# Optimization experiments

Hardware: AMD Instinct MI355X
Metric: run time of the kernel (lower is better)

## Reference

```python
import jax, jax.numpy as jnp
import numpy as np

K = 5          # retrieval_k
EPS = 1e-8     # torch cosine_similarity eps


def setup_inputs() -> dict:
    key = jax.random.key(0)
    ks = jax.random.split(key, 10)
    B, M, D, H = 1024, 65536, 384, 384
    return {
        "query": jax.random.normal(ks[0], (B, D), jnp.float32),
        "mem_vectors": jax.random.normal(ks[1], (M, D), jnp.float32),
        "coords": jax.random.normal(ks[2], (M, 2), jnp.float32),
        "spatial_weights": jax.random.normal(ks[3], (H, 2), jnp.float32),
        "W_ih": jax.random.normal(ks[4], (H, D), jnp.float32) * 0.05,
        "b_ih": jax.random.normal(ks[5], (H,), jnp.float32) * 0.05,
        "W_hh": jax.random.normal(ks[6], (H, H), jnp.float32) * 0.05,
        "b_hh": jax.random.normal(ks[7], (H,), jnp.float32) * 0.05,
        "W_g": jax.random.normal(ks[8], (H, D), jnp.float32) * 0.05,
        "b_g": jax.random.normal(ks[9], (H,), jnp.float32) * 0.05,
    }


def reference(query, mem_vectors, coords, spatial_weights,
              W_ih, b_ih, W_hh, b_hh, W_g, b_g):
    # --- spatial_activation: 1/(1+dist) from coords to mean of spatial_weights ---
    center = spatial_weights.mean(axis=0)                      # [2]
    dists = jnp.linalg.norm(coords - center, axis=1)           # [M]
    activations = 1.0 / (1.0 + dists)                          # [M]

    # --- retrieve_memories: cosine similarity + spatial activation, top-k ---
    qn = jnp.linalg.norm(query, axis=1, keepdims=True)         # [B,1]
    mn = jnp.linalg.norm(mem_vectors, axis=1, keepdims=True)   # [M,1]
    dots = query @ mem_vectors.T                               # [B,M]
    sim = dots / jnp.maximum(qn * mn.T, EPS)                   # cosine w/ torch eps
    total_sim = sim + activations[None, :]                     # [B,M]
    _, topk_idx = jax.lax.top_k(total_sim, K)                  # [B,K]
    retrieved = mem_vectors[topk_idx]                          # [B,K,D]

    # --- contextualize: tiny RNN over [query, retrieved...] then gated mix ---
    seq = jnp.concatenate([query[:, None, :], retrieved], axis=1)  # [B,K+1,D]
    x_proj = jnp.einsum('btd,hd->bth', seq, W_ih) + b_ih           # [B,K+1,H]

    def step(h, x_t):  # x_t: [B,H]
        h = jnp.tanh(x_t + h @ W_hh.T + b_hh)
        return h, None

    h0 = jnp.zeros((query.shape[0], W_hh.shape[0]), query.dtype)
    h, _ = jax.lax.scan(step, h0, jnp.swapaxes(x_proj, 0, 1))      # [B,H]

    gate = jax.nn.sigmoid(query @ W_g.T + b_g)                     # [B,H]
    direct = query @ W_ih.T + b_ih                                 # [B,H]
    return gate * h + (1.0 - gate) * direct
```

## Files before the change

kernel.cpp:

```cpp
#include <hip/hip_runtime.h>
#include <math.h>

namespace {

typedef float f32x4 __attribute__((ext_vector_type(4)));
typedef float f32x16 __attribute__((ext_vector_type(16)));
typedef short bf16x8 __attribute__((ext_vector_type(8)));
typedef unsigned short ushort_t;

constexpr int B  = 1024;
constexpr int M  = 65536;
constexpr int D  = 384;
constexpr int H  = 384;
constexpr int KK = 5;
constexpr int NC = 128;
constexpr int CHUNK = M / NC;
constexpr float FEPS = 1e-8f;

__device__ __forceinline__ ushort_t f2bf(float x) {
  unsigned int u = __float_as_uint(x);
  unsigned int r = (u + 0x7FFFu + ((u >> 16) & 1u)) >> 16;
  return (ushort_t)r;
}
__device__ __forceinline__ float bf2f(ushort_t h) {
  return __uint_as_float(((unsigned int)h) << 16);
}

__device__ __forceinline__ void async16(const ushort_t* g, ushort_t* l) {
  __builtin_amdgcn_global_load_lds(
      (const __attribute__((address_space(1))) unsigned int*)g,
      (__attribute__((address_space(3))) unsigned int*)l, 16, 0, 0);
}

__device__ __forceinline__ void insert3b(unsigned int* k, unsigned int v) {
  unsigned int t0 = min(k[0], v); k[0] = max(k[0], v);
  unsigned int t1 = min(k[1], t0); k[1] = max(k[1], t0);
  k[2] = max(k[2], t1);
}
__device__ __forceinline__ void insert5b(unsigned int* k, unsigned int v) {
  unsigned int t0 = min(k[0], v); k[0] = max(k[0], v);
  unsigned int t1 = min(k[1], t0); k[1] = max(k[1], t0);
  unsigned int t2 = min(k[2], t1); k[2] = max(k[2], t1);
  unsigned int t3 = min(k[3], t2); k[3] = max(k[3], t2);
  k[4] = max(k[4], t3);
}

__device__ __forceinline__ int swz_koff(int lane) {
  return (((lane & 3) ^ ((lane >> 3) & 3)) * 8);
}

__global__ __launch_bounds__(256) void k_prep(
    const float* __restrict__ q, const float* __restrict__ mem,
    const float* __restrict__ coords, const float* __restrict__ sw,
    const float* __restrict__ W_ih, const float* __restrict__ W_hh,
    const float* __restrict__ W_g,
    ushort_t* __restrict__ qh, ushort_t* __restrict__ mh,
    float2* __restrict__ f2a, float2* __restrict__ f2b,
    ushort_t* __restrict__ wihh, ushort_t* __restrict__ wihl,
    ushort_t* __restrict__ whhh, ushort_t* __restrict__ whhl,
    ushort_t* __restrict__ wgh, ushort_t* __restrict__ wgl) {
  int wv = threadIdx.x >> 6, lane = threadIdx.x & 63;
  int bid = blockIdx.x;
  if (bid < M/8) {
    int r0 = bid*8 + wv*2;
    float cx = 0.f, cy = 0.f;
    for (int i = lane; i < H; i += 64) { cx += sw[2*i]; cy += sw[2*i+1]; }
#pragma unroll
    for (int o = 32; o > 0; o >>= 1) { cx += __shfl_xor(cx, o); cy += __shfl_xor(cy, o); }
    cx *= (1.0f/384.0f); cy *= (1.0f/384.0f);
    float4 x[3]; float s0 = 0.f, s1 = 0.f;
#pragma unroll
    for (int k = 0; k < 3; ++k) {
      x[k] = ((const float4*)(mem + (size_t)r0*D))[lane + 64*k];
      float d = x[k].x*x[k].x + x[k].y*x[k].y + x[k].z*x[k].z + x[k].w*x[k].w;
      if (k == 0) s0 += d;
      else if (k == 2) s1 += d;
      else { if (lane < 32) s0 += d; else s1 += d; }
    }
#pragma unroll
    for (int o = 32; o > 0; o >>= 1) { s0 += __shfl_xor(s0, o); s1 += __shfl_xor(s1, o); }
#pragma unroll
    for (int k = 0; k < 3; ++k) {
      ushort4 hh;
      hh.x = f2bf(x[k].x); hh.y = f2bf(x[k].y);
      hh.z = f2bf(x[k].z); hh.w = f2bf(x[k].w);
      ((ushort4*)(mh + (size_t)r0*D))[lane + 64*k] = hh;
    }
    if (lane < 2) {
      int r = r0 + lane;
      float mn = sqrtf(lane == 0 ? s0 : s1);
      float dx = coords[2*r] - cx, dy = coords[2*r+1] - cy;
      float act = 1.0f / (1.0f + sqrtf(dx*dx + dy*dy));
      f2a[r] = make_float2(1.0f / mn, act + 2.0f);
      f2b[r] = make_float2(mn, act);
    }
  } else if (bid < M/8 + B/8) {
    int r0 = (bid - M/8)*8 + wv*2;
    float4 x[3]; float s0 = 0.f, s1 = 0.f;
#pragma unroll
    for (int k = 0; k < 3; ++k) {
      x[k] = ((const float4*)(q + (size_t)r0*D))[lane + 64*k];
      float d = x[k].x*x[k].x + x[k].y*x[k].y + x[k].z*x[k].z + x[k].w*x[k].w;
      if (k == 0) s0 += d;
      else if (k == 2) s1 += d;
      else { if (lane < 32) s0 += d; else s1 += d; }
    }
#pragma unroll
    for (int o = 32; o > 0; o >>= 1) { s0 += __shfl_xor(s0, o); s1 += __shfl_xor(s1, o); }
    float inv0 = 1.0f / sqrtf(s0), inv1 = 1.0f / sqrtf(s1);
#pragma unroll
    for (int k = 0; k < 3; ++k) {
      float sc = (k == 0) ? inv0 : (k == 2) ? inv1 : (lane < 32 ? inv0 : inv1);
      ushort4 nn;
      nn.x = f2bf(x[k].x * sc); nn.y = f2bf(x[k].y * sc);
      nn.z = f2bf(x[k].z * sc); nn.w = f2bf(x[k].w * sc);
      ((ushort4*)(qh + (size_t)r0*D))[lane + 64*k] = nn;
    }
  } else {
    int r = (bid - M/8 - B/8)*4 + wv;
    const float* src; ushort_t* dh; ushort_t* dl;
    if (r < 384)      { src = W_ih + (size_t)r*D;       dh = wihh + (size_t)r*D;       dl = wihl + (size_t)r*D; }
    else if (r < 768) { src = W_hh + (size_t)(r-384)*D; dh = whhh + (size_t)(r-384)*D; dl = whhl + (size_t)(r-384)*D; }
    else              { src = W_g  + (size_t)(r-768)*D; dh = wgh  + (size_t)(r-768)*D; dl = wgl  + (size_t)(r-768)*D; }
#pragma unroll
    for (int k = 0; k < 3; ++k) {
      float2 v = ((const float2*)src)[lane + 64*k];
      ushort_t h0 = f2bf(v.x), h1 = f2bf(v.y);
      ushort2 hh; hh.x = h0; hh.y = h1;
      ushort2 ll; ll.x = f2bf(v.x - bf2f(h0)); ll.y = f2bf(v.y - bf2f(h1));
      ((ushort2*)dh)[lane + 64*k] = hh;
      ((ushort2*)dl)[lane + 64*k] = ll;
    }
  }
}

__global__ __launch_bounds__(256, 4) void k_sim(
    const ushort_t* __restrict__ qh,
    const ushort_t* __restrict__ mh,
    const float2* __restrict__ f2a, unsigned int* __restrict__ keybuf) {
  __shared__ __align__(16) ushort_t sQh[2*4096];
  __shared__ __align__(16) ushort_t sMh[2*4096];
  __shared__ __align__(16) float2 sF[CHUNK];

  const int tid = threadIdx.x, lane = tid & 63, wave = tid >> 6;
  const int wr = wave >> 1, wc = wave & 1;
  const int l31 = lane & 31, half = lane >> 5;
  const int flat = blockIdx.x;
  const int k8 = flat & 7, qb = (flat >> 3) & 7, mgrp = flat >> 6;
  const int nc = (mgrp << 3) | k8;
  const int rowoff = lane >> 2, koff = swz_koff(lane);
  const int gsw = (l31 >> 1) & 3;
  const size_t qrow0 = (size_t)qb * 128;

  ((float4*)sF)[tid] = ((const float4*)(f2a + (size_t)nc * CHUNK))[tid];

  auto stage = [&](int buf, int mt, int k12) {
    const size_t mrow0 = (size_t)nc * CHUNK + (size_t)mt * 128;
    const int kt = k12 * 32;
#pragma unroll
    for (int n = 0; n < 4; ++n) {
      int f = wave*4 + n;
      int arr = f >> 3, slot = f & 7;
      const ushort_t* src = arr == 0 ? qh : mh;
      ushort_t* dst = (arr == 0 ? sQh : sMh) + buf*4096;
      size_t rowb = arr == 0 ? qrow0 : mrow0;
      async16(src + (rowb + slot*16 + rowoff)*D + kt + koff,
              dst + slot*512 + lane*8);
    }
  };

  unsigned int keys[2][3];
#pragma unroll
  for (int j = 0; j < 2; ++j) { keys[j][0] = 0; keys[j][1] = 0; keys[j][2] = 0; }

  stage(0, 0, 0);
  __syncthreads();

  int cur = 0;
  f32x16 acc[2][2];

  for (int mt = 0; mt < 4; ++mt) {
#pragma unroll
    for (int i = 0; i < 2; ++i)
#pragma unroll
      for (int j = 0; j < 2; ++j) acc[i][j] = (f32x16)0.0f;

#pragma unroll
    for (int k12 = 0; k12 < 12; ++k12) {
      const int nmt = (k12 == 11) ? mt + 1 : mt;
      const int nk = (k12 == 11) ? 0 : k12 + 1;
      if (nmt < 4) stage(cur ^ 1, nmt, nk);

      const int base = cur * 4096;
      bf16x8 ah[2][2], bh[2][2];
#pragma unroll
      for (int i = 0; i < 2; ++i)
#pragma unroll
        for (int s = 0; s < 2; ++s) {
          int gra = ((s*2 + half) ^ gsw) * 8;
          int ro = base + (wr*64 + i*32 + l31)*32 + gra;
          ah[i][s] = *(const bf16x8*)&sMh[ro];
          int co = base + (wc*64 + i*32 + l31)*32 + gra;
          bh[i][s] = *(const bf16x8*)&sQh[co];
        }
#pragma unroll
      for (int i = 0; i < 2; ++i)
#pragma unroll
        for (int j = 0; j < 2; ++j)
#pragma unroll
          for (int s = 0; s < 2; ++s)
            acc[i][j] = __builtin_amdgcn_mfma_f32_32x32x16_bf16(ah[i][s], bh[j][s], acc[i][j], 0, 0, 0);

      if (k12 == 11) {
#pragma unroll
        for (int i = 0; i < 2; ++i)
#pragma unroll
          for (int rg = 0; rg < 4; ++rg)
#pragma unroll
            for (int rr = 0; rr < 4; ++rr) {
              int rl = wr*64 + i*32 + half*4 + rr + 8*rg;
              float2 fa = sF[mt*128 + rl];
              unsigned int idx = (unsigned int)(((nc & 1) << 9) | (mt*128 + rl));
              float v0 = fmaf(acc[i][0][rg*4+rr], fa.x, fa.y);
              insert3b(keys[0], (__float_as_uint(v0) & 0xFFFFFC00u) | idx);
              float v1 = fmaf(acc[i][1][rg*4+rr], fa.x, fa.y);
              insert3b(keys[1], (__float_as_uint(v1) & 0xFFFFFC00u) | idx);
            }
      }

      __syncthreads();
      cur ^= 1;
    }
  }

#pragma unroll
  for (int j = 0; j < 2; ++j) {
    int q_local = wc*64 + j*32 + l31;
    int c = wr*2 + half;
    size_t off = ((size_t)(qb*128 + q_local) * NC + nc) * 12 + c*3;
    keybuf[off+0] = keys[j][0];
    keybuf[off+1] = keys[j][1];
    keybuf[off+2] = keys[j][2];
  }
}

__global__ __launch_bounds__(256) void k_merge(
    const unsigned int* __restrict__ keybuf,
    const float* __restrict__ query, const float* __restrict__ memv,
    const float2* __restrict__ f2b,
    ushort_t* __restrict__ xsh, ushort_t* __restrict__ xsl) {
  __shared__ int sCand[16];
  __shared__ float sSimv[16];
  __shared__ int sTop[KK];
  const int tid = threadIdx.x, lane = tid & 63, wave = tid >> 6;
  const int q = blockIdx.x;

  if (wave == 0) {
    const unsigned int* kb = keybuf + (size_t)q * (NC*12) + (size_t)lane * 24;
    unsigned int k5[5] = {0,0,0,0,0};
#pragma unroll
    for (int c = 0; c < 6; ++c) {
      uint4 v = *(const uint4*)(kb + c*4);
      insert5b(k5, v.x); insert5b(k5, v.y); insert5b(k5, v.z); insert5b(k5, v.w);
    }
#pragma unroll
    for (int p = 0; p < 16; ++p) {
      unsigned int bk = k5[0]; int blv = lane;
#pragma unroll
      for (int off = 1; off < 64; off <<= 1) {
        unsigned int ok = (unsigned int)__shfl_xor((int)bk, off);
        int ol = __shfl_xor(blv, off);
        if (ok > bk || (ok == bk && ol < blv)) { bk = ok; blv = ol; }
      }
      if (lane == blv) { k5[0]=k5[1]; k5[1]=k5[2]; k5[2]=k5[3]; k5[3]=k5[4]; k5[4]=0; }
      if (lane == 0) sCand[p] = (blv << 10) | (int)(bk & 1023u);
    }
  }
  __syncthreads();

  float qv[6]; float sq = 0.f;
#pragma unroll
  for (int k = 0; k < 6; ++k) { qv[k] = query[(size_t)q*D + lane + 64*k]; sq += qv[k]*qv[k]; }
#pragma unroll
  for (int o = 32; o > 0; o >>= 1) sq += __shfl_xor(sq, o);
  float qn = sqrtf(sq);

#pragma unroll
  for (int pp = 0; pp < 4; ++pp) {
    int p = wave*4 + pp;
    int mi = sCand[p];
    float d = 0.f;
#pragma unroll
    for (int k = 0; k < 6; ++k) d += qv[k] * memv[(size_t)mi*D + lane + 64*k];
#pragma unroll
    for (int o = 32; o > 0; o >>= 1) d += __shfl_xor(d, o);
    if (lane == 0) {
      float2 fb = f2b[mi];
      sSimv[p] = d / fmaxf(qn * fb.x, FEPS) + fb.y;
    }
  }
  __syncthreads();

  if (tid == 0) {
    float cv[16]; int ci[16];
#pragma unroll
    for (int p = 0; p < 16; ++p) { cv[p] = sSimv[p]; ci[p] = sCand[p]; }
    for (int s = 0; s < KK; ++s) {
      int best = -1; float bv = -1e30f; int bi = 0x7FFFFFFF;
      for (int p = 0; p < 16; ++p) {
        if (ci[p] < 0) continue;
        if (cv[p] > bv || (cv[p] == bv && ci[p] < bi)) { best = p; bv = cv[p]; bi = ci[p]; }
      }
      sTop[s] = ci[best];
      ci[best] = -1;
    }
  }
  __syncthreads();

#pragma unroll
  for (int rep = 0; rep < 2; ++rep) {
    int t = wave + rep*4;
    if (t < 6) {
      const float* src = (t == 0) ? (query + (size_t)q*D)
                                  : (memv + (size_t)sTop[t-1]*D);
      size_t g = (size_t)q*6 + t;
#pragma unroll
      for (int k = 0; k < 3; ++k) {
        float2 v = ((const float2*)src)[lane + 64*k];
        ushort_t h0 = f2bf(v.x), h1 = f2bf(v.y);
        ushort2 hh; hh.x = h0; hh.y = h1;
        ushort2 ll; ll.x = f2bf(v.x - bf2f(h0)); ll.y = f2bf(v.y - bf2f(h1));
        ((ushort2*)(xsh + g*D))[lane + 64*k] = hh;
        ((ushort2*)(xsl + g*D))[lane + 64*k] = ll;
      }
    }
  }
}

__global__ __launch_bounds__(256) void k_tail1(
    const ushort_t* __restrict__ xsh, const ushort_t* __restrict__ xsl,
    const ushort_t* __restrict__ wihh, const ushort_t* __restrict__ wihl,
    const ushort_t* __restrict__ wgh, const ushort_t* __restrict__ wgl,
    const float* __restrict__ b_ih, const float* __restrict__ b_hh,
    const float* __restrict__ b_g,
    float* __restrict__ xp, float* __restrict__ gate,
    ushort_t* __restrict__ hoh, ushort_t* __restrict__ hol) {
  __shared__ __align__(16) ushort_t sAh[64*128];
  __shared__ __align__(16) ushort_t sAl[64*128];
  __shared__ __align__(16) ushort_t sWh[64*128];
  __shared__ __align__(16) ushort_t sWl[64*128];

  const int tid = threadIdx.x, lane = tid & 63, wave = tid >> 6;
  const int wr = wave >> 1, wc = wave & 1;
  const int t = lane & 15, quad = lane >> 4;
  const bool xmode = blockIdx.x < 96;
  const int cbase = blockIdx.y * 64;
  const int rowoff = lane >> 2, koff = swz_koff(lane);
  const int pq = (quad ^ ((t >> 1) & 3)) * 8;

  const ushort_t* gp[4];
  if (wave < 2) {
    const ushort_t* base = (wave == 0) ? xsh : xsl;
#pragma unroll
    for (int slot = 0; slot < 4; ++slot) {
      int rl = slot*16 + rowoff;
      size_t row = xmode ? (size_t)(blockIdx.x*64 + rl)
                         : (size_t)((blockIdx.x - 96)*64 + rl) * 6;
      gp[slot] = base + row*D + koff;
    }
  } else {
#pragma unroll
    for (int slot = 0; slot < 4; ++slot) {
      int rl = slot*16 + rowoff;
      const ushort_t* wsrc = xmode ? (wave == 2 ? wihh : wihl)
                                   : (wave == 2 ? wgh  : wgl);
      gp[slot] = wsrc + (size_t)(cbase + rl) * D + koff;
    }
  }
  ushort_t* ldst = (wave == 0) ? sAh : (wave == 1) ? sAl : (wave == 2) ? sWh : sWl;

  f32x4 acc[2][2];
#pragma unroll
  for (int i = 0; i < 2; ++i)
#pragma unroll
    for (int j = 0; j < 2; ++j) acc[i][j] = (f32x4)0.0f;

  for (int r3 = 0; r3 < 3; ++r3) {
    __syncthreads();
#pragma unroll
    for (int s = 0; s < 4; ++s)
#pragma unroll
      for (int slot = 0; slot < 4; ++slot)
        async16(gp[slot] + r3*128 + s*32, ldst + s*2048 + slot*512 + lane*8);
    __syncthreads();
#pragma unroll
    for (int s = 0; s < 4; ++s) {
      bf16x8 ah[2], al[2], bh[2], bl[2];
#pragma unroll
      for (int i = 0; i < 2; ++i) {
        int ro = s*2048 + (wr*32 + i*16 + t)*32 + pq;
        ah[i] = *(const bf16x8*)&sAh[ro];
        al[i] = *(const bf16x8*)&sAl[ro];
        int co = s*2048 + (wc*32 + i*16 + t)*32 + pq;
        bh[i] = *(const bf16x8*)&sWh[co];
        bl[i] = *(const bf16x8*)&sWl[co];
      }
#pragma unroll
      for (int i = 0; i < 2; ++i)
#pragma unroll
        for (int j = 0; j < 2; ++j) {
          acc[i][j] = __builtin_amdgcn_mfma_f32_16x16x32_bf16(ah[i], bh[j], acc[i][j], 0, 0, 0);
          acc[i][j] = __builtin_amdgcn_mfma_f32_16x16x32_bf16(ah[i], bl[j], acc[i][j], 0, 0, 0);
          acc[i][j] = __builtin_amdgcn_mfma_f32_16x16x32_bf16(al[i], bh[j], acc[i][j], 0, 0, 0);
        }
    }
  }

#pragma unroll
  for (int i = 0; i < 2; ++i)
#pragma unroll
    for (int j = 0; j < 2; ++j)
#pragma unroll
      for (int r = 0; r < 4; ++r) {
        int rloc = wr*32 + i*16 + quad*4 + r;
        int h = cbase + wc*32 + j*16 + t;
        float a = acc[i][j][r];
        if (xmode) {
          int g = blockIdx.x*64 + rloc;
          float v = a + b_ih[h];
          xp[(size_t)g*H + h] = v;
          int b = g / 6;
          if (g - b*6 == 0) {
            float hv = tanhf(v + b_hh[h]);
            ushort_t hi = f2bf(hv);
            hoh[(size_t)b*H + h] = hi;
            hol[(size_t)b*H + h] = f2bf(hv - bf2f(hi));
          }
        } else {
          int rq = (blockIdx.x - 96)*64 + rloc;
          gate[(size_t)rq*H + h] = 1.0f / (1.0f + expf(-(a + b_g[h])));
        }
      }
}

template<int LAST>
__global__ __launch_bounds__(256) void k_rnn(
    const ushort_t* __restrict__ hih, const ushort_t* __restrict__ hil,
    const ushort_t* __restrict__ whhh, const ushort_t* __restrict__ whhl,
    const float* __restrict__ b_hh, const float* __restrict__ xp,
    const float* __restrict__ gate, int step,
    ushort_t* __restrict__ hoh, ushort_t* __restrict__ hol,
    float* __restrict__ out) {
  __shared__ __align__(16) ushort_t sAh[32*128];
  __shared__ __align__(16) ushort_t sAl[32*128];
  __shared__ __align__(16) ushort_t sWh[64*128];
  __shared__ __align__(16) ushort_t sWl[64*128];

  const int tid = threadIdx.x, lane = tid & 63, wave = tid >> 6;
  const int wr = wave >> 1, wc = wave & 1;
  const int t = lane & 15, quad = lane >> 4;
  const int rbase = blockIdx.x * 32, cbase = blockIdx.y * 64;
  const int rowoff = lane >> 2, koff = swz_koff(lane);
  const int pq = (quad ^ ((t >> 1) & 3)) * 8;
  const int nslot = (wave < 2) ? 2 : 4;
  const int sstride = (wave < 2) ? 1024 : 2048;

  const ushort_t* gp[4];
#pragma unroll
  for (int slot = 0; slot < 4; ++slot) {
    int rl = slot*16 + rowoff;
    const ushort_t* src =
        (wave == 0) ? hih + (size_t)(rbase + rl)*D :
        (wave == 1) ? hil + (size_t)(rbase + rl)*D :
        (wave == 2) ? whhh + (size_t)(cbase + rl)*D :
                      whhl + (size_t)(cbase + rl)*D;
    gp[slot] = src + koff;
  }
  ushort_t* ldst = (wave == 0) ? sAh : (wave == 1) ? sAl : (wave == 2) ? sWh : sWl;

  f32x4 acc[2];
#pragma unroll
  for (int j = 0; j < 2; ++j) acc[j] = (f32x4)0.0f;

  for (int r3 = 0; r3 < 3; ++r3) {
    __syncthreads();
#pragma unroll
    for (int s = 0; s < 4; ++s)
      for (int slot = 0; slot < nslot; ++slot)
        async16(gp[slot] + r3*128 + s*32, ldst + s*sstride + slot*512 + lane*8);
    __syncthreads();
#pragma unroll
    for (int s = 0; s < 4; ++s) {
      int ro = s*1024 + (wr*16 + t)*32 + pq;
      bf16x8 ah = *(const bf16x8*)&sAh[ro];
      bf16x8 al = *(const bf16x8*)&sAl[ro];
      bf16x8 bh[2], bl[2];
#pragma unroll
      for (int j = 0; j < 2; ++j) {
        int co = s*2048 + (wc*32 + j*16 + t)*32 + pq;
        bh[j] = *(const bf16x8*)&sWh[co];
        bl[j] = *(const bf16x8*)&sWl[co];
      }
#pragma unroll
      for (int j = 0; j < 2; ++j) {
        acc[j] = __builtin_amdgcn_mfma_f32_16x16x32_bf16(ah, bh[j], acc[j], 0, 0, 0);
        acc[j] = __builtin_amdgcn_mfma_f32_16x16x32_bf16(ah, bl[j], acc[j], 0, 0, 0);
        acc[j] = __builtin_amdgcn_mfma_f32_16x16x32_bf16(al, bh[j], acc[j], 0, 0, 0);
      }
    }
  }

#pragma unroll
  for (int j = 0; j < 2; ++j)
#pragma unroll
    for (int r = 0; r < 4; ++r) {
      int row = rbase + wr*16 + quad*4 + r;
      int h = cbase + wc*32 + j*16 + t;
      float v = acc[j][r] + b_hh[h] + xp[(size_t)row*(6*H) + step*H + h];
      float hv = tanhf(v);
      if (LAST) {
        float g = gate[(size_t)row*H + h];
        out[(size_t)row*H + h] = g*hv + (1.0f - g)*xp[(size_t)row*(6*H) + h];
      } else {
        ushort_t hi = f2bf(hv);
        hoh[(size_t)row*H + h] = hi;
        hol[(size_t)row*H + h] = f2bf(hv - bf2f(hi));
      }
    }
}

}

extern "C" void kernel_launch(void* const* d_in, const int* in_sizes, int n_in,
                              void* d_out, int out_size, void* d_ws, size_t ws_size,
                              hipStream_t stream) {
  const float* query = (const float*)d_in[0];
  const float* memv  = (const float*)d_in[1];
  const float* coords= (const float*)d_in[2];
  const float* sw    = (const float*)d_in[3];
  const float* W_ih  = (const float*)d_in[4];
  const float* b_ih  = (const float*)d_in[5];
  const float* W_hh  = (const float*)d_in[6];
  const float* b_hh  = (const float*)d_in[7];
  const float* W_g   = (const float*)d_in[8];
  const float* b_g   = (const float*)d_in[9];
  float* out = (float*)d_out;

  char* p = (char*)d_ws;
  auto alloc = [&](size_t bytes) {
    char* r = p; p += (bytes + 255) & ~(size_t)255; return r;
  };
  ushort_t* qh  = (ushort_t*)alloc((size_t)B * D * 2);
  ushort_t* mh  = (ushort_t*)alloc((size_t)M * D * 2);
  float2* f2a   = (float2*)alloc((size_t)M * 8);
  float2* f2b   = (float2*)alloc((size_t)M * 8);
  ushort_t* wihh = (ushort_t*)alloc((size_t)H * D * 2);
  ushort_t* wihl = (ushort_t*)alloc((size_t)H * D * 2);
  ushort_t* whhh = (ushort_t*)alloc((size_t)H * D * 2);
  ushort_t* whhl = (ushort_t*)alloc((size_t)H * D * 2);
  ushort_t* wgh  = (ushort_t*)alloc((size_t)H * D * 2);
  ushort_t* wgl  = (ushort_t*)alloc((size_t)H * D * 2);
  unsigned int* keybuf = (unsigned int*)alloc((size_t)B * NC * 12 * 4);
  ushort_t* xsh = (ushort_t*)alloc((size_t)B * 6 * D * 2);
  ushort_t* xsl = (ushort_t*)alloc((size_t)B * 6 * D * 2);
  float* xp     = (float*)alloc((size_t)B * 6 * H * 4);
  float* gate   = (float*)alloc((size_t)B * H * 4);
  ushort_t* hAh = (ushort_t*)alloc((size_t)B * H * 2);
  ushort_t* hAl = (ushort_t*)alloc((size_t)B * H * 2);
  ushort_t* hBh = (ushort_t*)alloc((size_t)B * H * 2);
  ushort_t* hBl = (ushort_t*)alloc((size_t)B * H * 2);

  k_prep<<<M/8 + B/8 + 288, 256, 0, stream>>>(
      query, memv, coords, sw, W_ih, W_hh, W_g,
      qh, mh, f2a, f2b,
      wihh, wihl, whhh, whhl, wgh, wgl);
  k_sim<<<1024, 256, 0, stream>>>(qh, mh, f2a, keybuf);
  k_merge<<<B, 256, 0, stream>>>(keybuf, query, memv, f2b, xsh, xsl);
  k_tail1<<<dim3(112, 6), 256, 0, stream>>>(
      xsh, xsl, wihh, wihl, wgh, wgl,
      b_ih, b_hh, b_g, xp, gate, hAh, hAl);
  k_rnn<0><<<dim3(32, 6), 256, 0, stream>>>(hAh, hAl, whhh, whhl, b_hh, xp, gate, 1, hBh, hBl, out);
  k_rnn<0><<<dim3(32, 6), 256, 0, stream>>>(hBh, hBl, whhh, whhl, b_hh, xp, gate, 2, hAh, hAl, out);
  k_rnn<0><<<dim3(32, 6), 256, 0, stream>>>(hAh, hAl, whhh, whhl, b_hh, xp, gate, 3, hBh, hBl, out);
  k_rnn<0><<<dim3(32, 6), 256, 0, stream>>>(hBh, hBl, whhh, whhl, b_hh, xp, gate, 4, hAh, hAl, out);
  k_rnn<1><<<dim3(32, 6), 256, 0, stream>>>(hAh, hAl, whhh, whhl, b_hh, xp, gate, 5, hBh, hBl, out);
}
```

Measured before the change: 330.1 us.

## Enlarge sim tile to 256 memory rows per block stage

The similarity GEMM block tile grows from 128x128 to 256 memory rows x 128 queries. Each wave now computes a 128x64 sub-tile with 8 MFMA accumulators, so every loaded query fragment is reused across twice as many memory rows. This halves the number of outer m-tile iterations and the barriers they carry. In exchange it doubles accumulator registers and the memory-row LDS buffer, and launch bounds drop to 2 blocks per CU, lowering occupancy.

```diff
diff --git a/kernel.cpp b/kernel.cpp
--- a/kernel.cpp
+++ b/kernel.cpp
@@ -134,12 +134,12 @@
   }
 }
 
-__global__ __launch_bounds__(256, 4) void k_sim(
+__global__ __launch_bounds__(256, 2) void k_sim(
     const ushort_t* __restrict__ qh,
     const ushort_t* __restrict__ mh,
     const float2* __restrict__ f2a, unsigned int* __restrict__ keybuf) {
+  __shared__ __align__(16) ushort_t sMh[2*8192];
   __shared__ __align__(16) ushort_t sQh[2*4096];
-  __shared__ __align__(16) ushort_t sMh[2*4096];
   __shared__ __align__(16) float2 sF[CHUNK];
 
   const int tid = threadIdx.x, lane = tid & 63, wave = tid >> 6;
@@ -154,16 +154,17 @@
 
   ((float4*)sF)[tid] = ((const float4*)(f2a + (size_t)nc * CHUNK))[tid];
 
-  auto stage = [&](int buf, int mt, int k12) {
-    const size_t mrow0 = (size_t)nc * CHUNK + (size_t)mt * 128;
+  auto stage = [&](int buf, int pair, int k12) {
+    const size_t mrow0 = (size_t)nc * CHUNK + (size_t)pair * 256;
     const int kt = k12 * 32;
 #pragma unroll
-    for (int n = 0; n < 4; ++n) {
-      int f = wave*4 + n;
-      int arr = f >> 3, slot = f & 7;
-      const ushort_t* src = arr == 0 ? qh : mh;
-      ushort_t* dst = (arr == 0 ? sQh : sMh) + buf*4096;
-      size_t rowb = arr == 0 ? qrow0 : mrow0;
+    for (int n = 0; n < 6; ++n) {
+      int f = wave*6 + n;
+      bool isQ = f >= 16;
+      int slot = isQ ? (f - 16) : f;
+      const ushort_t* src = isQ ? qh : mh;
+      ushort_t* dst = isQ ? (sQh + buf*4096) : (sMh + buf*8192);
+      size_t rowb = isQ ? qrow0 : mrow0;
       async16(src + (rowb + slot*16 + rowoff)*D + kt + koff,
               dst + slot*512 + lane*8);
     }
@@ -177,34 +178,38 @@
   __syncthreads();
 
   int cur = 0;
-  f32x16 acc[2][2];
-
-  for (int mt = 0; mt < 4; ++mt) {
-#pragma unroll
-    for (int i = 0; i < 2; ++i)
+  f32x16 acc[4][2];
+
+  for (int pair = 0; pair < 2; ++pair) {
+#pragma unroll
+    for (int i = 0; i < 4; ++i)
 #pragma unroll
       for (int j = 0; j < 2; ++j) acc[i][j] = (f32x16)0.0f;
 
 #pragma unroll
     for (int k12 = 0; k12 < 12; ++k12) {
-      const int nmt = (k12 == 11) ? mt + 1 : mt;
+      const int npair = (k12 == 11) ? pair + 1 : pair;
       const int nk = (k12 == 11) ? 0 : k12 + 1;
-      if (nmt < 4) stage(cur ^ 1, nmt, nk);
-
-      const int base = cur * 4096;
-      bf16x8 ah[2][2], bh[2][2];
-#pragma unroll
-      for (int i = 0; i < 2; ++i)
-#pragma unroll
-        for (int s = 0; s < 2; ++s) {
-          int gra = ((s*2 + half) ^ gsw) * 8;
-          int ro = base + (wr*64 + i*32 + l31)*32 + gra;
+      if (npair < 2) stage(cur ^ 1, npair, nk);
+
+      const int mbase = cur * 8192, qbase = cur * 4096;
+      bf16x8 ah[4][2], bh[2][2];
+#pragma unroll
+      for (int s = 0; s < 2; ++s) {
+        int gra = ((s*2 + half) ^ gsw) * 8;
+#pragma unroll
+        for (int i = 0; i < 4; ++i) {
+          int ro = mbase + (wr*128 + i*32 + l31)*32 + gra;
           ah[i][s] = *(const bf16x8*)&sMh[ro];
-          int co = base + (wc*64 + i*32 + l31)*32 + gra;
-          bh[i][s] = *(const bf16x8*)&sQh[co];
         }
 #pragma unroll
-      for (int i = 0; i < 2; ++i)
+        for (int j = 0; j < 2; ++j) {
+          int co = qbase + (wc*64 + j*32 + l31)*32 + gra;
+          bh[j][s] = *(const bf16x8*)&sQh[co];
+        }
+      }
+#pragma unroll
+      for (int i = 0; i < 4; ++i)
 #pragma unroll
         for (int j = 0; j < 2; ++j)
 #pragma unroll
@@ -213,14 +218,14 @@
 
       if (k12 == 11) {
 #pragma unroll
-        for (int i = 0; i < 2; ++i)
+        for (int i = 0; i < 4; ++i)
 #pragma unroll
           for (int rg = 0; rg < 4; ++rg)
 #pragma unroll
             for (int rr = 0; rr < 4; ++rr) {
-              int rl = wr*64 + i*32 + half*4 + rr + 8*rg;
-              float2 fa = sF[mt*128 + rl];
-              unsigned int idx = (unsigned int)(((nc & 1) << 9) | (mt*128 + rl));
+              int rl = wr*128 + i*32 + half*4 + rr + 8*rg;
+              float2 fa = sF[pair*256 + rl];
+              unsigned int idx = (unsigned int)(((nc & 1) << 9) | (pair*256 + rl));
               float v0 = fmaf(acc[i][0][rg*4+rr], fa.x, fa.y);
               insert3b(keys[0], (__float_as_uint(v0) & 0xFFFFFC00u) | idx);
               float v1 = fmaf(acc[i][1][rg*4+rr], fa.x, fa.y);
```

Result: no change. 326.1 us (-1.2%).
